# Performance work log

Measured on AMD Instinct MI355X. Metric: run time of the kernel, lower is better.

Reference implementation:

```python
import jax, jax.numpy as jnp
import numpy as np

N_NODES = 100000
N_EDGES = 1600000
IN_DIM = 128
OUT_DIM = 64
EDGE_DIM = 8


def setup_inputs() -> dict:
    key = jax.random.key(0)
    ks = jax.random.split(key, 7)
    h = jax.random.normal(ks[0], (N_NODES, IN_DIM), dtype=jnp.float32)
    edge_index = jax.random.randint(ks[1], (2, N_EDGES), 0, N_NODES, dtype=jnp.int64)
    edge_attr = jax.random.normal(ks[2], (N_EDGES, EDGE_DIM), dtype=jnp.float32)
    w_w = jax.random.normal(ks[3], (IN_DIM, OUT_DIM), dtype=jnp.float32) * (1.0 / np.sqrt(IN_DIM))
    w_b = jax.random.normal(ks[4], (OUT_DIM,), dtype=jnp.float32) * 0.01
    a_w = jax.random.normal(ks[5], (2 * OUT_DIM + EDGE_DIM, 1), dtype=jnp.float32) * 0.1
    a_b = jax.random.normal(ks[6], (1,), dtype=jnp.float32) * 0.01
    return {"h": h, "edge_index": edge_index, "edge_attr": edge_attr,
            "w_w": w_w, "w_b": w_b, "a_w": a_w, "a_b": a_b}


def reference(h, edge_index, edge_attr, w_w, w_b, a_w, a_b):
    n = h.shape[0]
    d = w_w.shape[1]
    wh = h @ w_w + w_b                              # [N, out_dim]
    row, col = edge_index[0], edge_index[1]
    # a([wh[row], wh[col], edge_attr]) == wh[row]@a1 + wh[col]@a2 + edge_attr@a3 + b
    a1, a2, a3 = a_w[:d], a_w[d:2 * d], a_w[2 * d:]
    s_row = wh @ a1                                 # [N, 1] per-node attention terms
    s_col = wh @ a2                                 # [N, 1]
    e = jax.nn.leaky_relu(s_row[row] + s_col[col] + edge_attr @ a3 + a_b)  # [E, 1]
    # segment softmax over edges grouped by destination `row`
    max_e = jax.ops.segment_max(e, row, num_segments=n)     # [N, 1]
    alpha = jnp.exp(e - max_e[row])                          # [E, 1]
    out = jax.ops.segment_sum(alpha * wh[col], row, num_segments=n)  # [N, out_dim]
    norm = jax.ops.segment_sum(alpha, row, num_segments=n)           # [N, 1]
    return out / (norm + 1e-8)
```

## Files before the change

kernel.cpp:

```cpp
#include <hip/hip_runtime.h>
#include <hip/hip_fp16.h>

#define IN_DIM 128
#define OUT_DIM 64
#define RPB 512
#define MAXB 200
#define EPB 2048

typedef __attribute__((ext_vector_type(8))) _Float16 half8;
typedef __attribute__((ext_vector_type(4))) float f32x4;

__global__ __launch_bounds__(256) void k_wh(
    const float* __restrict__ h, const float* __restrict__ w_w,
    const float* __restrict__ w_b, const float* __restrict__ a_w,
    __half* __restrict__ wh, float* __restrict__ s_row,
    float* __restrict__ s_col, int n_nodes) {
  __shared__ _Float16 wf[4 * 4 * 64 * 8];
  for (int idx = threadIdx.x; idx < IN_DIM * OUT_DIM; idx += 256) {
    int k = idx >> 6, c = idx & 63;
    int mt = c >> 4;
    int kt = k >> 5;
    int l = (((k >> 3) & 3) << 4) | (c & 15);
    int j = k & 7;
    wf[(((mt << 2) | kt) << 9) | (l << 3) | j] = (_Float16)w_w[idx];
  }
  __syncthreads();

  const int lane = threadIdx.x & 63;
  const int wv = threadIdx.x >> 6;

  half8 A[4][4];
#pragma unroll
  for (int mt = 0; mt < 4; ++mt)
#pragma unroll
    for (int kt = 0; kt < 4; ++kt)
      A[mt][kt] =
          *(const half8*)&wf[(((mt << 2) | kt) << 9) | (lane << 3)];

  const int cbase = (lane >> 4) << 2;
  f32x4 bq[4], a1q[4], a2q[4];
#pragma unroll
  for (int mt = 0; mt < 4; ++mt) {
    bq[mt] = *(const f32x4*)&w_b[mt * 16 + cbase];
    a1q[mt] = *(const f32x4*)&a_w[mt * 16 + cbase];
    a2q[mt] = *(const f32x4*)&a_w[OUT_DIM + mt * 16 + cbase];
  }

  const int ntiles = (n_nodes + 15) >> 4;
  const int tstride = gridDim.x << 2;
  for (int t = blockIdx.x * 4 + wv; t < ntiles; t += tstride) {
    const int n0 = t << 4;
    const int node = n0 + (lane & 15);
    const int nodec = node < n_nodes ? node : n_nodes - 1;
    const float4* hv =
        (const float4*)(h + (size_t)nodec * IN_DIM + ((lane >> 4) << 3));
    float4 p[8];
#pragma unroll
    for (int kt = 0; kt < 4; ++kt) {
      p[2 * kt] = hv[kt * 8];
      p[2 * kt + 1] = hv[kt * 8 + 1];
    }
    f32x4 C[4];
#pragma unroll
    for (int mt = 0; mt < 4; ++mt) C[mt] = (f32x4){0.f, 0.f, 0.f, 0.f};
#pragma unroll
    for (int kt = 0; kt < 4; ++kt) {
      const float4 u = p[2 * kt], v = p[2 * kt + 1];
      half8 B;
      B[0] = (_Float16)u.x; B[1] = (_Float16)u.y;
      B[2] = (_Float16)u.z; B[3] = (_Float16)u.w;
      B[4] = (_Float16)v.x; B[5] = (_Float16)v.y;
      B[6] = (_Float16)v.z; B[7] = (_Float16)v.w;
#pragma unroll
      for (int mt = 0; mt < 4; ++mt)
        C[mt] = __builtin_amdgcn_mfma_f32_16x16x32_f16(A[mt][kt], B, C[mt],
                                                       0, 0, 0);
    }
    float sr = 0.f, sc = 0.f;
    uint2 q[4];
#pragma unroll
    for (int mt = 0; mt < 4; ++mt) {
      f32x4 d = C[mt] + bq[mt];
      sr += d[0] * a1q[mt][0] + d[1] * a1q[mt][1] + d[2] * a1q[mt][2] +
            d[3] * a1q[mt][3];
      sc += d[0] * a2q[mt][0] + d[1] * a2q[mt][1] + d[2] * a2q[mt][2] +
            d[3] * a2q[mt][3];
      __half2 lo = __floats2half2_rn(d[0], d[1]);
      __half2 hi = __floats2half2_rn(d[2], d[3]);
      q[mt].x = *(unsigned int*)&lo;
      q[mt].y = *(unsigned int*)&hi;
    }
    if (node < n_nodes) {
      uint2* wrow = (uint2*)(wh + (size_t)node * OUT_DIM + cbase);
      wrow[0] = q[0];
      wrow[4] = q[1];
      wrow[8] = q[2];
      wrow[12] = q[3];
    }
    sr += __shfl_xor(sr, 16, 64);
    sr += __shfl_xor(sr, 32, 64);
    sc += __shfl_xor(sc, 16, 64);
    sc += __shfl_xor(sc, 32, 64);
    if (lane < 16 && node < n_nodes) {
      s_row[node] = sr;
      s_col[node] = sc;
    }
  }
}

__global__ __launch_bounds__(512) void k_pre(
    const int* __restrict__ ei, int* __restrict__ blockhist, int nedges) {
  __shared__ int hist[MAXB];
  for (int b = threadIdx.x; b < MAXB; b += 512) hist[b] = 0;
  __syncthreads();
  const int e0 = blockIdx.x * EPB;
  if (e0 + EPB <= nedges) {
    const int e = e0 + threadIdx.x;
    int r0 = ei[e];
    int r1 = ei[e + 512];
    int r2 = ei[e + 1024];
    int r3 = ei[e + 1536];
    atomicAdd(&hist[r0 >> 9], 1);
    atomicAdd(&hist[r1 >> 9], 1);
    atomicAdd(&hist[r2 >> 9], 1);
    atomicAdd(&hist[r3 >> 9], 1);
  } else {
#pragma unroll
    for (int r = 0; r < EPB / 512; ++r) {
      int e = e0 + r * 512 + threadIdx.x;
      if (e < nedges) atomicAdd(&hist[ei[e] >> 9], 1);
    }
  }
  __syncthreads();
  for (int b = threadIdx.x; b < MAXB; b += 512)
    blockhist[blockIdx.x * MAXB + b] = hist[b];
}

__global__ __launch_bounds__(512) void k_scanA(
    const int* __restrict__ blockhist, int* __restrict__ boff,
    int* __restrict__ cnt, int nbl) {
  __shared__ int sd[512];
  const int b = blockIdx.x, t = threadIdx.x;
  int i0 = 2 * t, i1 = 2 * t + 1;
  int v0 = (i0 < nbl) ? ((blockhist[i0 * MAXB + b] + 7) & ~7) : 0;
  int v1 = (i1 < nbl) ? ((blockhist[i1 * MAXB + b] + 7) & ~7) : 0;
  int ts = v0 + v1;
  sd[t] = ts;
  __syncthreads();
  for (int off = 1; off < 512; off <<= 1) {
    int x = (t >= off) ? sd[t - off] : 0;
    __syncthreads();
    sd[t] += x;
    __syncthreads();
  }
  int excl = sd[t] - ts;
  if (i0 < nbl) boff[i0 * MAXB + b] = excl;
  if (i1 < nbl) boff[i1 * MAXB + b] = excl + v0;
  if (t == 511) cnt[b] = sd[511];
}

__global__ __launch_bounds__(256) void k_scanB(
    const int* __restrict__ cnt, int* __restrict__ bbase, int nb) {
  __shared__ int sd[256];
  int t = threadIdx.x;
  int pc = (t < nb) ? ((cnt[t] + 15) & ~15) : 0;
  sd[t] = pc;
  __syncthreads();
  for (int off = 1; off < 256; off <<= 1) {
    int x = (t >= off) ? sd[t - off] : 0;
    __syncthreads();
    sd[t] += x;
    __syncthreads();
  }
  if (t < nb) bbase[t] = sd[t] - pc;
}

__global__ __launch_bounds__(512) void k_fill(
    const int* __restrict__ ei, const float* __restrict__ edge_attr,
    const float* __restrict__ a_w, const float* __restrict__ a_b,
    const float* __restrict__ s_row, const float* __restrict__ s_col,
    const int* __restrict__ boff, const int* __restrict__ bbase,
    int2* __restrict__ entA, int nedges, int nb) {
  __shared__ int cur[MAXB];
  for (int b = threadIdx.x; b < MAXB; b += 512)
    cur[b] = (b < nb) ? bbase[b] + boff[blockIdx.x * MAXB + b] : 0;
  float aw0 = a_w[128], aw1 = a_w[129], aw2 = a_w[130], aw3 = a_w[131];
  float aw4 = a_w[132], aw5 = a_w[133], aw6 = a_w[134], aw7 = a_w[135];
  float ab = a_b[0];
  __syncthreads();
  const int e0 = blockIdx.x * EPB;
  if (e0 + EPB <= nedges) {
    const int e = e0 + threadIdx.x;
    int row[4], col[4];
#pragma unroll
    for (int r = 0; r < 4; ++r) {
      row[r] = ei[e + r * 512];
      col[r] = ei[nedges + e + r * 512];
    }
    float4 u[4], v[4];
#pragma unroll
    for (int r = 0; r < 4; ++r) {
      const float4* ea = (const float4*)(edge_attr + (size_t)(e + r * 512) * 8);
      u[r] = ea[0];
      v[r] = ea[1];
    }
    float sr[4], sc[4];
#pragma unroll
    for (int r = 0; r < 4; ++r) {
      sr[r] = s_row[row[r]];
      sc[r] = s_col[col[r]];
    }
#pragma unroll
    for (int r = 0; r < 4; ++r) {
      float s = sr[r] + sc[r] + ab;
      s += u[r].x * aw0 + u[r].y * aw1 + u[r].z * aw2 + u[r].w * aw3;
      s += v[r].x * aw4 + v[r].y * aw5 + v[r].z * aw6 + v[r].w * aw7;
      float ev = (s > 0.f) ? s : 0.01f * s;
      float alpha = __expf(ev);
      int pos = atomicAdd(&cur[row[r] >> 9], 1);
      entA[pos] =
          make_int2(((row[r] & 511) << 17) | col[r], __float_as_int(alpha));
    }
  } else {
    for (int r = 0; r < EPB / 512; ++r) {
      int e = e0 + r * 512 + threadIdx.x;
      if (e < nedges) {
        int row = ei[e];
        int col = ei[nedges + e];
        const float4* ea = (const float4*)(edge_attr + (size_t)e * 8);
        float4 u = ea[0], v = ea[1];
        float s = s_row[row] + s_col[col] + ab;
        s += u.x * aw0 + u.y * aw1 + u.z * aw2 + u.w * aw3;
        s += v.x * aw4 + v.y * aw5 + v.z * aw6 + v.w * aw7;
        float ev = (s > 0.f) ? s : 0.01f * s;
        float alpha = __expf(ev);
        int pos = atomicAdd(&cur[row >> 9], 1);
        entA[pos] = make_int2(((row & 511) << 17) | col, __float_as_int(alpha));
      }
    }
  }
  __syncthreads();
  for (int b = threadIdx.x; b < nb; b += 512) {
    int c = cur[b], end = (c + 7) & ~7;
    for (int k = c; k < end; ++k) entA[k] = make_int2(-1, 0);
  }
}

__global__ __launch_bounds__(512) void k_sortb(
    const int2* __restrict__ entA, int2* __restrict__ entB,
    const int* __restrict__ cnt, const int* __restrict__ bbase,
    int* __restrict__ nodeoffs, int* __restrict__ nodecnt, int n_nodes) {
  __shared__ int hist[RPB];
  __shared__ int loffs[RPB];
  __shared__ int cur[RPB];
  const int b = blockIdx.x, t = threadIdx.x;
  const int c = cnt[b];
  const int base = bbase[b];
  const int row0 = b << 9;
  hist[t] = 0;
  __syncthreads();
  for (int i = t; i < c; i += 512) {
    int x = entA[base + i].x;
    if (x >= 0) atomicAdd(&hist[x >> 17], 1);
  }
  __syncthreads();
  int hh = hist[t];
  loffs[t] = hh;
  __syncthreads();
  for (int off = 1; off < 512; off <<= 1) {
    int x = (t >= off) ? loffs[t - off] : 0;
    __syncthreads();
    loffs[t] += x;
    __syncthreads();
  }
  int excl = loffs[t] - hh;
  cur[t] = excl;
  int node = row0 + t;
  if (node < n_nodes) {
    nodeoffs[node] = base + excl;
    nodecnt[node] = hh;
  }
  __syncthreads();
  for (int i = t; i < c; i += 512) {
    int2 p = entA[base + i];
    if (p.x >= 0) {
      int pos = atomicAdd(&cur[p.x >> 17], 1);
      entB[base + pos] = p;
    }
  }
}

__global__ __launch_bounds__(256) void k_agg(
    const int* __restrict__ nodeoffs, const int* __restrict__ nodecnt,
    const int2* __restrict__ ent, const __half* __restrict__ wh,
    float* __restrict__ out, int n_nodes) {
  int v = blockIdx.x * 4 + (threadIdx.x >> 6);
  if (v >= n_nodes) return;
  const int lane = threadIdx.x & 63;
  const int slot = lane >> 3, sub = lane & 7;
  const int start = __builtin_amdgcn_readfirstlane(nodeoffs[v]);
  const int deg = __builtin_amdgcn_readfirstlane(nodecnt[v]);
  const uint4* whq = (const uint4*)wh;
  float acc[8] = {0.f, 0.f, 0.f, 0.f, 0.f, 0.f, 0.f, 0.f};
  float l = 0.f;
  for (int base = 0; base < deg; base += 16) {
    const int i0 = base + slot, i1 = base + 8 + slot;
    const bool g0 = i0 < deg, g1 = i1 < deg;
    int2 p0 = make_int2(0, 0), p1 = make_int2(0, 0);
    if (g0) p0 = ent[start + i0];
    if (g1) p1 = ent[start + i1];
    uint4 q0 = make_uint4(0, 0, 0, 0), q1 = make_uint4(0, 0, 0, 0);
    if (g0) q0 = whq[(size_t)(p0.x & 0x1FFFF) * 8 + sub];
    if (g1) q1 = whq[(size_t)(p1.x & 0x1FFFF) * 8 + sub];
    if (g0) {
      float a = __int_as_float(p0.y);
      float2 f0 = __half22float2(*(__half2*)&q0.x);
      float2 f1 = __half22float2(*(__half2*)&q0.y);
      float2 f2 = __half22float2(*(__half2*)&q0.z);
      float2 f3 = __half22float2(*(__half2*)&q0.w);
      acc[0] = fmaf(a, f0.x, acc[0]); acc[1] = fmaf(a, f0.y, acc[1]);
      acc[2] = fmaf(a, f1.x, acc[2]); acc[3] = fmaf(a, f1.y, acc[3]);
      acc[4] = fmaf(a, f2.x, acc[4]); acc[5] = fmaf(a, f2.y, acc[5]);
      acc[6] = fmaf(a, f3.x, acc[6]); acc[7] = fmaf(a, f3.y, acc[7]);
      if (sub == 0) l += a;
    }
    if (g1) {
      float a = __int_as_float(p1.y);
      float2 f0 = __half22float2(*(__half2*)&q1.x);
      float2 f1 = __half22float2(*(__half2*)&q1.y);
      float2 f2 = __half22float2(*(__half2*)&q1.z);
      float2 f3 = __half22float2(*(__half2*)&q1.w);
      acc[0] = fmaf(a, f0.x, acc[0]); acc[1] = fmaf(a, f0.y, acc[1]);
      acc[2] = fmaf(a, f1.x, acc[2]); acc[3] = fmaf(a, f1.y, acc[3]);
      acc[4] = fmaf(a, f2.x, acc[4]); acc[5] = fmaf(a, f2.y, acc[5]);
      acc[6] = fmaf(a, f3.x, acc[6]); acc[7] = fmaf(a, f3.y, acc[7]);
      if (sub == 0) l += a;
    }
  }
#pragma unroll
  for (int c = 0; c < 8; ++c) {
    acc[c] += __shfl_xor(acc[c], 8, 64);
    acc[c] += __shfl_xor(acc[c], 16, 64);
    acc[c] += __shfl_xor(acc[c], 32, 64);
  }
  l += __shfl_xor(l, 8, 64);
  l += __shfl_xor(l, 16, 64);
  l += __shfl_xor(l, 32, 64);
  float lt = __shfl(l, 0, 64);
  if (slot == 0) {
    float inv = 1.0f / (lt + 1e-8f);
    float4 o0 = make_float4(acc[0] * inv, acc[1] * inv, acc[2] * inv,
                            acc[3] * inv);
    float4 o1 = make_float4(acc[4] * inv, acc[5] * inv, acc[6] * inv,
                            acc[7] * inv);
    float4* orow = (float4*)out + (size_t)v * 16 + sub * 2;
    orow[0] = o0;
    orow[1] = o1;
  }
}

extern "C" void kernel_launch(void* const* d_in, const int* in_sizes, int n_in,
                              void* d_out, int out_size, void* d_ws, size_t ws_size,
                              hipStream_t stream) {
  const float* h         = (const float*)d_in[0];
  const int*   ei        = (const int*)d_in[1];
  const float* edge_attr = (const float*)d_in[2];
  const float* w_w       = (const float*)d_in[3];
  const float* w_b       = (const float*)d_in[4];
  const float* a_w       = (const float*)d_in[5];
  const float* a_b       = (const float*)d_in[6];
  const int n_nodes = in_sizes[0] / IN_DIM;
  const int nedges  = in_sizes[1] / 2;
  const int nb   = (n_nodes + RPB - 1) / RPB;
  const int nebl = (nedges + EPB - 1) / EPB;

  const size_t entcap = (size_t)nedges + (size_t)nebl * nb * 8 + (size_t)nb * 16;

  __half* wh       = (__half*)d_ws;
  int2*  entA      = (int2*)(wh + (size_t)n_nodes * OUT_DIM);
  int*   cnt       = (int*)(entA + entcap);
  int*   bbase     = cnt + MAXB;
  int*   nodeoffs  = bbase + MAXB;
  int*   nodecnt   = nodeoffs + n_nodes;
  int2*  entB      = (int2*)(nodecnt + n_nodes);
  float* s_row     = (float*)entB;
  float* s_col     = s_row + n_nodes;
  int*   blockhist = (int*)(s_col + n_nodes);
  int*   boff      = blockhist + (size_t)nebl * MAXB;

  k_wh<<<640, 256, 0, stream>>>(h, w_w, w_b, a_w, wh, s_row, s_col, n_nodes);
  k_pre<<<nebl, 512, 0, stream>>>(ei, blockhist, nedges);
  k_scanA<<<nb, 512, 0, stream>>>(blockhist, boff, cnt, nebl);
  k_scanB<<<1, 256, 0, stream>>>(cnt, bbase, nb);
  k_fill<<<nebl, 512, 0, stream>>>(ei, edge_attr, a_w, a_b, s_row, s_col,
                                   boff, bbase, entA, nedges, nb);
  k_sortb<<<nb, 512, 0, stream>>>(entA, entB, cnt, bbase, nodeoffs, nodecnt, n_nodes);
  k_agg<<<(n_nodes + 3) / 4, 256, 0, stream>>>(nodeoffs, nodecnt, entB, wh,
                                               (float*)d_out, n_nodes);
}
```

Before: 272.9 us.

## Fuse per-row sort into aggregation with LDS-staged 128-row buckets

```diff
diff --git a/kernel.cpp b/kernel.cpp
--- a/kernel.cpp
+++ b/kernel.cpp
@@ -3,9 +3,10 @@
 
 #define IN_DIM 128
 #define OUT_DIM 64
-#define RPB 512
-#define MAXB 200
-#define EPB 2048
+#define RPB 128
+#define MAXB 800
+#define EPB 4096
+#define ENTL 2304
 
 typedef __attribute__((ext_vector_type(8))) _Float16 half8;
 typedef __attribute__((ext_vector_type(4))) float f32x4;
@@ -116,19 +117,16 @@
   const int e0 = blockIdx.x * EPB;
   if (e0 + EPB <= nedges) {
     const int e = e0 + threadIdx.x;
-    int r0 = ei[e];
-    int r1 = ei[e + 512];
-    int r2 = ei[e + 1024];
-    int r3 = ei[e + 1536];
-    atomicAdd(&hist[r0 >> 9], 1);
-    atomicAdd(&hist[r1 >> 9], 1);
-    atomicAdd(&hist[r2 >> 9], 1);
-    atomicAdd(&hist[r3 >> 9], 1);
+    int r[8];
+#pragma unroll
+    for (int k = 0; k < 8; ++k) r[k] = ei[e + k * 512];
+#pragma unroll
+    for (int k = 0; k < 8; ++k) atomicAdd(&hist[r[k] >> 7], 1);
   } else {
 #pragma unroll
-    for (int r = 0; r < EPB / 512; ++r) {
-      int e = e0 + r * 512 + threadIdx.x;
-      if (e < nedges) atomicAdd(&hist[ei[e] >> 9], 1);
+    for (int k = 0; k < 8; ++k) {
+      int e = e0 + k * 512 + threadIdx.x;
+      if (e < nedges) atomicAdd(&hist[ei[e] >> 7], 1);
     }
   }
   __syncthreads();
@@ -159,26 +157,30 @@
   if (t == 511) cnt[b] = sd[511];
 }
 
-__global__ __launch_bounds__(256) void k_scanB(
+__global__ __launch_bounds__(512) void k_scanB(
     const int* __restrict__ cnt, int* __restrict__ bbase, int nb) {
-  __shared__ int sd[256];
+  __shared__ int sd[512];
   int t = threadIdx.x;
-  int pc = (t < nb) ? ((cnt[t] + 15) & ~15) : 0;
-  sd[t] = pc;
-  __syncthreads();
-  for (int off = 1; off < 256; off <<= 1) {
+  int i0 = 2 * t, i1 = 2 * t + 1;
+  int v0 = (i0 < nb) ? ((cnt[i0] + 15) & ~15) : 0;
+  int v1 = (i1 < nb) ? ((cnt[i1] + 15) & ~15) : 0;
+  int ts = v0 + v1;
+  sd[t] = ts;
+  __syncthreads();
+  for (int off = 1; off < 512; off <<= 1) {
     int x = (t >= off) ? sd[t - off] : 0;
     __syncthreads();
     sd[t] += x;
     __syncthreads();
   }
-  if (t < nb) bbase[t] = sd[t] - pc;
+  int excl = sd[t] - ts;
+  if (i0 < nb) bbase[i0] = excl;
+  if (i1 < nb) bbase[i1] = excl + v0;
 }
 
 __global__ __launch_bounds__(512) void k_fill(
     const int* __restrict__ ei, const float* __restrict__ edge_attr,
-    const float* __restrict__ a_w, const float* __restrict__ a_b,
-    const float* __restrict__ s_row, const float* __restrict__ s_col,
+    const float* __restrict__ a_w,
     const int* __restrict__ boff, const int* __restrict__ bbase,
     int2* __restrict__ entA, int nedges, int nb) {
   __shared__ int cur[MAXB];
@@ -186,56 +188,47 @@
     cur[b] = (b < nb) ? bbase[b] + boff[blockIdx.x * MAXB + b] : 0;
   float aw0 = a_w[128], aw1 = a_w[129], aw2 = a_w[130], aw3 = a_w[131];
   float aw4 = a_w[132], aw5 = a_w[133], aw6 = a_w[134], aw7 = a_w[135];
-  float ab = a_b[0];
   __syncthreads();
   const int e0 = blockIdx.x * EPB;
   if (e0 + EPB <= nedges) {
-    const int e = e0 + threadIdx.x;
-    int row[4], col[4];
-#pragma unroll
-    for (int r = 0; r < 4; ++r) {
-      row[r] = ei[e + r * 512];
-      col[r] = ei[nedges + e + r * 512];
-    }
-    float4 u[4], v[4];
-#pragma unroll
-    for (int r = 0; r < 4; ++r) {
-      const float4* ea = (const float4*)(edge_attr + (size_t)(e + r * 512) * 8);
-      u[r] = ea[0];
-      v[r] = ea[1];
-    }
-    float sr[4], sc[4];
-#pragma unroll
-    for (int r = 0; r < 4; ++r) {
-      sr[r] = s_row[row[r]];
-      sc[r] = s_col[col[r]];
-    }
-#pragma unroll
-    for (int r = 0; r < 4; ++r) {
-      float s = sr[r] + sc[r] + ab;
-      s += u[r].x * aw0 + u[r].y * aw1 + u[r].z * aw2 + u[r].w * aw3;
-      s += v[r].x * aw4 + v[r].y * aw5 + v[r].z * aw6 + v[r].w * aw7;
-      float ev = (s > 0.f) ? s : 0.01f * s;
-      float alpha = __expf(ev);
-      int pos = atomicAdd(&cur[row[r] >> 9], 1);
-      entA[pos] =
-          make_int2(((row[r] & 511) << 17) | col[r], __float_as_int(alpha));
+#pragma unroll
+    for (int g = 0; g < 2; ++g) {
+      const int e = e0 + g * 2048 + threadIdx.x;
+      int row[4], col[4];
+#pragma unroll
+      for (int r = 0; r < 4; ++r) {
+        row[r] = ei[e + r * 512];
+        col[r] = ei[nedges + e + r * 512];
+      }
+      float4 u[4], v[4];
+#pragma unroll
+      for (int r = 0; r < 4; ++r) {
+        const float4* ea =
+            (const float4*)(edge_attr + (size_t)(e + r * 512) * 8);
+        u[r] = ea[0];
+        v[r] = ea[1];
+      }
+#pragma unroll
+      for (int r = 0; r < 4; ++r) {
+        float s = u[r].x * aw0 + u[r].y * aw1 + u[r].z * aw2 + u[r].w * aw3;
+        s += v[r].x * aw4 + v[r].y * aw5 + v[r].z * aw6 + v[r].w * aw7;
+        int pos = atomicAdd(&cur[row[r] >> 7], 1);
+        entA[pos] =
+            make_int2(((row[r] & 127) << 17) | col[r], __float_as_int(s));
+      }
     }
   } else {
-    for (int r = 0; r < EPB / 512; ++r) {
-      int e = e0 + r * 512 + threadIdx.x;
+    for (int k = 0; k < 8; ++k) {
+      int e = e0 + k * 512 + threadIdx.x;
       if (e < nedges) {
         int row = ei[e];
         int col = ei[nedges + e];
         const float4* ea = (const float4*)(edge_attr + (size_t)e * 8);
         float4 u = ea[0], v = ea[1];
-        float s = s_row[row] + s_col[col] + ab;
-        s += u.x * aw0 + u.y * aw1 + u.z * aw2 + u.w * aw3;
+        float s = u.x * aw0 + u.y * aw1 + u.z * aw2 + u.w * aw3;
         s += v.x * aw4 + v.y * aw5 + v.z * aw6 + v.w * aw7;
-        float ev = (s > 0.f) ? s : 0.01f * s;
-        float alpha = __expf(ev);
-        int pos = atomicAdd(&cur[row >> 9], 1);
-        entA[pos] = make_int2(((row & 511) << 17) | col, __float_as_int(alpha));
+        int pos = atomicAdd(&cur[row >> 7], 1);
+        entA[pos] = make_int2(((row & 127) << 17) | col, __float_as_int(s));
       }
     }
   }
@@ -246,116 +239,137 @@
   }
 }
 
-__global__ __launch_bounds__(512) void k_sortb(
-    const int2* __restrict__ entA, int2* __restrict__ entB,
-    const int* __restrict__ cnt, const int* __restrict__ bbase,
-    int* __restrict__ nodeoffs, int* __restrict__ nodecnt, int n_nodes) {
-  __shared__ int hist[RPB];
-  __shared__ int loffs[RPB];
-  __shared__ int cur[RPB];
-  const int b = blockIdx.x, t = threadIdx.x;
+__global__ __launch_bounds__(512) void k_sagg(
+    const int2* __restrict__ entA, const int* __restrict__ cnt,
+    const int* __restrict__ bbase, const __half* __restrict__ wh,
+    const float* __restrict__ s_row, const float* __restrict__ s_col,
+    const float* __restrict__ a_b, float* __restrict__ out, int n_nodes) {
+  __shared__ int2 entl[ENTL];
+  __shared__ int hist[RPB], sd[RPB], starts[RPB], curs[RPB], degs[RPB];
+  const int b = blockIdx.x;
+  const int row0 = b << 7;
+  const int t = threadIdx.x;
+  if (t < RPB) hist[t] = 0;
+  __syncthreads();
   const int c = cnt[b];
   const int base = bbase[b];
-  const int row0 = b << 9;
-  hist[t] = 0;
-  __syncthreads();
-  for (int i = t; i < c; i += 512) {
-    int x = entA[base + i].x;
-    if (x >= 0) atomicAdd(&hist[x >> 17], 1);
-  }
-  __syncthreads();
-  int hh = hist[t];
-  loffs[t] = hh;
-  __syncthreads();
-  for (int off = 1; off < 512; off <<= 1) {
-    int x = (t >= off) ? loffs[t - off] : 0;
-    __syncthreads();
-    loffs[t] += x;
-    __syncthreads();
-  }
-  int excl = loffs[t] - hh;
-  cur[t] = excl;
-  int node = row0 + t;
-  if (node < n_nodes) {
-    nodeoffs[node] = base + excl;
-    nodecnt[node] = hh;
-  }
-  __syncthreads();
-  for (int i = t; i < c; i += 512) {
+  int2 e[8];
+#pragma unroll
+  for (int k = 0; k < 8; ++k) {
+    int i = t + k * 512;
+    e[k] = (i < c) ? entA[base + i] : make_int2(-1, 0);
+  }
+#pragma unroll
+  for (int k = 0; k < 8; ++k)
+    if (e[k].x >= 0) atomicAdd(&hist[e[k].x >> 17], 1);
+  for (int i = t + 4096; i < c; i += 512) {
     int2 p = entA[base + i];
-    if (p.x >= 0) {
-      int pos = atomicAdd(&cur[p.x >> 17], 1);
-      entB[base + pos] = p;
-    }
-  }
-}
-
-__global__ __launch_bounds__(256) void k_agg(
-    const int* __restrict__ nodeoffs, const int* __restrict__ nodecnt,
-    const int2* __restrict__ ent, const __half* __restrict__ wh,
-    float* __restrict__ out, int n_nodes) {
-  int v = blockIdx.x * 4 + (threadIdx.x >> 6);
-  if (v >= n_nodes) return;
-  const int lane = threadIdx.x & 63;
+    if (p.x >= 0) atomicAdd(&hist[p.x >> 17], 1);
+  }
+  __syncthreads();
+  int hh = 0;
+  if (t < RPB) { hh = hist[t]; sd[t] = hh; }
+  __syncthreads();
+  for (int off = 1; off < RPB; off <<= 1) {
+    int x = (t >= off && t < RPB) ? sd[t - off] : 0;
+    __syncthreads();
+    if (t < RPB) sd[t] += x;
+    __syncthreads();
+  }
+  if (t < RPB) {
+    int excl = sd[t] - hh;
+    starts[t] = excl;
+    curs[t] = excl;
+    degs[t] = hh;
+  }
+  __syncthreads();
+#pragma unroll
+  for (int k = 0; k < 8; ++k)
+    if (e[k].x >= 0) {
+      int p = atomicAdd(&curs[e[k].x >> 17], 1);
+      if (p < ENTL) entl[p] = e[k];
+    }
+  for (int i = t + 4096; i < c; i += 512) {
+    int2 p2 = entA[base + i];
+    if (p2.x >= 0) {
+      int p = atomicAdd(&curs[p2.x >> 17], 1);
+      if (p < ENTL) entl[p] = p2;
+    }
+  }
+  __syncthreads();
+  const int wv = t >> 6;
+  const int lane = t & 63;
   const int slot = lane >> 3, sub = lane & 7;
-  const int start = __builtin_amdgcn_readfirstlane(nodeoffs[v]);
-  const int deg = __builtin_amdgcn_readfirstlane(nodecnt[v]);
+  const float ab = a_b[0];
   const uint4* whq = (const uint4*)wh;
-  float acc[8] = {0.f, 0.f, 0.f, 0.f, 0.f, 0.f, 0.f, 0.f};
-  float l = 0.f;
-  for (int base = 0; base < deg; base += 16) {
-    const int i0 = base + slot, i1 = base + 8 + slot;
-    const bool g0 = i0 < deg, g1 = i1 < deg;
-    int2 p0 = make_int2(0, 0), p1 = make_int2(0, 0);
-    if (g0) p0 = ent[start + i0];
-    if (g1) p1 = ent[start + i1];
-    uint4 q0 = make_uint4(0, 0, 0, 0), q1 = make_uint4(0, 0, 0, 0);
-    if (g0) q0 = whq[(size_t)(p0.x & 0x1FFFF) * 8 + sub];
-    if (g1) q1 = whq[(size_t)(p1.x & 0x1FFFF) * 8 + sub];
-    if (g0) {
-      float a = __int_as_float(p0.y);
-      float2 f0 = __half22float2(*(__half2*)&q0.x);
-      float2 f1 = __half22float2(*(__half2*)&q0.y);
-      float2 f2 = __half22float2(*(__half2*)&q0.z);
-      float2 f3 = __half22float2(*(__half2*)&q0.w);
-      acc[0] = fmaf(a, f0.x, acc[0]); acc[1] = fmaf(a, f0.y, acc[1]);
-      acc[2] = fmaf(a, f1.x, acc[2]); acc[3] = fmaf(a, f1.y, acc[3]);
-      acc[4] = fmaf(a, f2.x, acc[4]); acc[5] = fmaf(a, f2.y, acc[5]);
-      acc[6] = fmaf(a, f3.x, acc[6]); acc[7] = fmaf(a, f3.y, acc[7]);
-      if (sub == 0) l += a;
-    }
-    if (g1) {
-      float a = __int_as_float(p1.y);
-      float2 f0 = __half22float2(*(__half2*)&q1.x);
-      float2 f1 = __half22float2(*(__half2*)&q1.y);
-      float2 f2 = __half22float2(*(__half2*)&q1.z);
-      float2 f3 = __half22float2(*(__half2*)&q1.w);
-      acc[0] = fmaf(a, f0.x, acc[0]); acc[1] = fmaf(a, f0.y, acc[1]);
-      acc[2] = fmaf(a, f1.x, acc[2]); acc[3] = fmaf(a, f1.y, acc[3]);
-      acc[4] = fmaf(a, f2.x, acc[4]); acc[5] = fmaf(a, f2.y, acc[5]);
-      acc[6] = fmaf(a, f3.x, acc[6]); acc[7] = fmaf(a, f3.y, acc[7]);
-      if (sub == 0) l += a;
-    }
-  }
-#pragma unroll
-  for (int c = 0; c < 8; ++c) {
-    acc[c] += __shfl_xor(acc[c], 8, 64);
-    acc[c] += __shfl_xor(acc[c], 16, 64);
-    acc[c] += __shfl_xor(acc[c], 32, 64);
-  }
-  l += __shfl_xor(l, 8, 64);
-  l += __shfl_xor(l, 16, 64);
-  l += __shfl_xor(l, 32, 64);
-  float lt = __shfl(l, 0, 64);
-  if (slot == 0) {
-    float inv = 1.0f / (lt + 1e-8f);
-    float4 o0 = make_float4(acc[0] * inv, acc[1] * inv, acc[2] * inv,
-                            acc[3] * inv);
-    float4 o1 = make_float4(acc[4] * inv, acc[5] * inv, acc[6] * inv,
-                            acc[7] * inv);
-    float4* orow = (float4*)out + (size_t)v * 16 + sub * 2;
-    orow[0] = o0;
-    orow[1] = o1;
+  for (int j = 0; j < 16; ++j) {
+    const int rl = wv * 16 + j;
+    const int node = row0 + rl;
+    if (node >= n_nodes) break;
+    const int st = starts[rl];
+    const int dg = degs[rl];
+    const float sab = s_row[node] + ab;
+    float acc[8] = {0.f, 0.f, 0.f, 0.f, 0.f, 0.f, 0.f, 0.f};
+    float l = 0.f;
+    for (int bas = 0; bas < dg; bas += 16) {
+      const int i0 = bas + slot, i1 = bas + 8 + slot;
+      const bool g0 = i0 < dg, g1 = i1 < dg;
+      int2 p0 = g0 ? entl[st + i0] : make_int2(0, 0);
+      int2 p1 = g1 ? entl[st + i1] : make_int2(0, 0);
+      const int col0 = p0.x & 0x1FFFF, col1 = p1.x & 0x1FFFF;
+      uint4 q0 = make_uint4(0, 0, 0, 0), q1 = make_uint4(0, 0, 0, 0);
+      float sc0 = 0.f, sc1 = 0.f;
+      if (g0) { q0 = whq[(size_t)col0 * 8 + sub]; sc0 = s_col[col0]; }
+      if (g1) { q1 = whq[(size_t)col1 * 8 + sub]; sc1 = s_col[col1]; }
+      if (g0) {
+        float s = sab + sc0 + __int_as_float(p0.y);
+        float ev = (s > 0.f) ? s : 0.01f * s;
+        float a = __expf(ev);
+        float2 f0 = __half22float2(*(__half2*)&q0.x);
+        float2 f1 = __half22float2(*(__half2*)&q0.y);
+        float2 f2 = __half22float2(*(__half2*)&q0.z);
+        float2 f3 = __half22float2(*(__half2*)&q0.w);
+        acc[0] = fmaf(a, f0.x, acc[0]); acc[1] = fmaf(a, f0.y, acc[1]);
+        acc[2] = fmaf(a, f1.x, acc[2]); acc[3] = fmaf(a, f1.y, acc[3]);
+        acc[4] = fmaf(a, f2.x, acc[4]); acc[5] = fmaf(a, f2.y, acc[5]);
+        acc[6] = fmaf(a, f3.x, acc[6]); acc[7] = fmaf(a, f3.y, acc[7]);
+        if (sub == 0) l += a;
+      }
+      if (g1) {
+        float s = sab + sc1 + __int_as_float(p1.y);
+        float ev = (s > 0.f) ? s : 0.01f * s;
+        float a = __expf(ev);
+        float2 f0 = __half22float2(*(__half2*)&q1.x);
+        float2 f1 = __half22float2(*(__half2*)&q1.y);
+        float2 f2 = __half22float2(*(__half2*)&q1.z);
+        float2 f3 = __half22float2(*(__half2*)&q1.w);
+        acc[0] = fmaf(a, f0.x, acc[0]); acc[1] = fmaf(a, f0.y, acc[1]);
+        acc[2] = fmaf(a, f1.x, acc[2]); acc[3] = fmaf(a, f1.y, acc[3]);
+        acc[4] = fmaf(a, f2.x, acc[4]); acc[5] = fmaf(a, f2.y, acc[5]);
+        acc[6] = fmaf(a, f3.x, acc[6]); acc[7] = fmaf(a, f3.y, acc[7]);
+        if (sub == 0) l += a;
+      }
+    }
+#pragma unroll
+    for (int d = 0; d < 8; ++d) {
+      acc[d] += __shfl_xor(acc[d], 8, 64);
+      acc[d] += __shfl_xor(acc[d], 16, 64);
+      acc[d] += __shfl_xor(acc[d], 32, 64);
+    }
+    l += __shfl_xor(l, 8, 64);
+    l += __shfl_xor(l, 16, 64);
+    l += __shfl_xor(l, 32, 64);
+    float lt = __shfl(l, 0, 64);
+    if (slot == 0) {
+      float inv = 1.0f / (lt + 1e-8f);
+      float4 o0 = make_float4(acc[0] * inv, acc[1] * inv, acc[2] * inv,
+                              acc[3] * inv);
+      float4 o1 = make_float4(acc[4] * inv, acc[5] * inv, acc[6] * inv,
+                              acc[7] * inv);
+      float4* orow = (float4*)out + (size_t)node * 16 + sub * 2;
+      orow[0] = o0;
+      orow[1] = o1;
+    }
   }
 }
 
@@ -380,10 +394,7 @@
   int2*  entA      = (int2*)(wh + (size_t)n_nodes * OUT_DIM);
   int*   cnt       = (int*)(entA + entcap);
   int*   bbase     = cnt + MAXB;
-  int*   nodeoffs  = bbase + MAXB;
-  int*   nodecnt   = nodeoffs + n_nodes;
-  int2*  entB      = (int2*)(nodecnt + n_nodes);
-  float* s_row     = (float*)entB;
+  float* s_row     = (float*)(bbase + MAXB);
   float* s_col     = s_row + n_nodes;
   int*   blockhist = (int*)(s_col + n_nodes);
   int*   boff      = blockhist + (size_t)nebl * MAXB;
@@ -391,10 +402,9 @@
   k_wh<<<640, 256, 0, stream>>>(h, w_w, w_b, a_w, wh, s_row, s_col, n_nodes);
   k_pre<<<nebl, 512, 0, stream>>>(ei, blockhist, nedges);
   k_scanA<<<nb, 512, 0, stream>>>(blockhist, boff, cnt, nebl);
-  k_scanB<<<1, 256, 0, stream>>>(cnt, bbase, nb);
-  k_fill<<<nebl, 512, 0, stream>>>(ei, edge_attr, a_w, a_b, s_row, s_col,
-                                   boff, bbase, entA, nedges, nb);
-  k_sortb<<<nb, 512, 0, stream>>>(entA, entB, cnt, bbase, nodeoffs, nodecnt, n_nodes);
-  k_agg<<<(n_nodes + 3) / 4, 256, 0, stream>>>(nodeoffs, nodecnt, entB, wh,
-                                               (float*)d_out, n_nodes);
-}
+  k_scanB<<<1, 512, 0, stream>>>(cnt, bbase, nb);
+  k_fill<<<nebl, 512, 0, stream>>>(ei, edge_attr, a_w, boff, bbase, entA,
+                                   nedges, nb);
+  k_sagg<<<nb, 512, 0, stream>>>(entA, cnt, bbase, wh, s_row, s_col, a_b,
+                                 (float*)d_out, n_nodes);
+}
```

After: 255.4 us. 6.4% less time.
